# Kernel tuning notes

Measured on AMD Instinct MI355X. Metric: run time of the kernel, lower is better.

Reference implementation:

```python
import jax, jax.numpy as jnp
import numpy as np

J = 3
J_H = 5
C_IN = 128
C_OUT = 128
N0, N1, N2 = 1024, 3072, 2048
DENSITY = 0.01
W_SCALE = 0.02  # keeps P^(2^(J_h-1)) @ x @ W magnitudes reasonable in fp32


def _sym_sparse(key, n, density):
    kv, km = jax.random.split(key)
    mask = jax.random.uniform(km, (n, n)) < density
    a = jnp.where(mask, jax.random.normal(kv, (n, n)), 0.0)
    return jnp.triu(a) + jnp.triu(a, 1).T  # symmetric sparse 'Laplacian'


def _sparse(kv, km, shape, density):
    mask = jax.random.uniform(km, shape) < density
    return jnp.where(mask, jax.random.normal(kv, shape), 0.0)


def setup_inputs() -> dict:
    key = jax.random.key(0)
    ks = jax.random.split(key, 24)
    z0 = jax.random.normal(ks[0], (N0, C_IN), jnp.float32)
    z1 = jax.random.normal(ks[1], (N1, C_IN), jnp.float32)
    z2 = jax.random.normal(ks[2], (N2, C_IN), jnp.float32)
    L0 = _sym_sparse(ks[3], N0, 0.02)
    L1_d = _sym_sparse(ks[4], N1, DENSITY)
    L1_u = _sym_sparse(ks[5], N1, DENSITY)
    L2 = _sym_sparse(ks[6], N2, DENSITY)
    B1 = _sparse(ks[7], ks[8], (N0, N1), DENSITY)
    B2 = _sparse(ks[9], ks[10], (N1, N2), DENSITY)
    W_d = jax.random.normal(ks[11], (J, C_IN, C_OUT)) * W_SCALE
    W_u = jax.random.normal(ks[12], (J, C_IN, C_OUT)) * W_SCALE
    W_h = jax.random.normal(ks[13], (C_IN, C_OUT)) * W_SCALE
    W_b1 = jax.random.normal(ks[14], (J, C_IN, C_OUT)) * W_SCALE
    W_b2 = jax.random.normal(ks[15], (J, C_IN, C_OUT)) * W_SCALE
    attn_d_w = jax.random.normal(ks[16], (1, 2 * C_IN)) * W_SCALE
    attn_d_b = jax.random.normal(ks[17], (1,)) * W_SCALE
    attn_u_w = jax.random.normal(ks[18], (1, 2 * C_IN)) * W_SCALE
    attn_u_b = jax.random.normal(ks[19], (1,)) * W_SCALE
    return dict(z0=z0, z1=z1, z2=z2, L0=L0, L1_d=L1_d, L1_u=L1_u, L2=L2,
                B1=B1, B2=B2, W_d=W_d, W_u=W_u, W_h=W_h, W_b1=W_b1, W_b2=W_b2,
                attn_d_w=attn_d_w, attn_d_b=attn_d_b,
                attn_u_w=attn_u_w, attn_u_b=attn_u_b)


def _attention(x, n, w, b, src, dst):
    # gather edge endpoints -> tiny MLP -> sigmoid -> symmetric scatter
    a = jnp.concatenate([x[src], x[dst]], axis=-1)      # [E, 2C]
    s = jax.nn.sigmoid(a @ w.T + b)[:, 0]               # [E]
    return jnp.zeros((n, n), x.dtype).at[src, dst].set(s).at[dst, src].set(s)


def _harmonic(L, x, W_h):
    lmax = jnp.linalg.eigvalsh(L)[-1]
    # torch does lambda_max.item() -> constant w.r.t. grads
    eps = jax.lax.stop_gradient(jnp.where(lmax > 0, 1.0 / lmax, 0.1))
    P = jnp.eye(L.shape[0], dtype=x.dtype) - eps * L
    for _ in range(J_H - 1):
        P = P @ P                                        # P^(2^(J_h-1))
    return P @ x @ W_h


def reference(z0, z1, z2, L0, L1_d, L1_u, L2, B1, B2,
              W_d, W_u, W_h, W_b1, W_b2,
              attn_d_w, attn_d_b, attn_u_w, attn_u_b):
    # nonzero patterns of the Laplacians (constants, computed on host)
    src_d, dst_d = np.nonzero(np.asarray(jax.device_get(L1_d)))
    src_u, dst_u = np.nonzero(np.asarray(jax.device_get(L1_u)))
    L1d_attn = _attention(z1, N1, attn_d_w, attn_d_b,
                          jnp.asarray(src_d), jnp.asarray(dst_d))
    L1u_attn = _attention(z1, N1, attn_u_w, attn_u_b,
                          jnp.asarray(src_u), jnp.asarray(dst_u))
    # sum_j (A @ z) @ W[j] == (A @ z) @ W.sum(0)
    Wd_s, Wu_s = W_d.sum(0), W_u.sum(0)
    Wb1_s, Wb2_s = W_b1.sum(0), W_b2.sum(0)

    z0_out = (L0 @ z0) @ Wd_s + (B1 @ z1) @ Wb1_s + _harmonic(L0, z0, W_h)
    z0_out = jax.nn.relu(z0_out)

    z1_out = ((L1d_attn @ z1) @ Wd_s + (L1u_attn @ z1) @ Wu_s
              + (B1.T @ z0) @ Wb1_s + (B2 @ z2) @ Wb2_s
              + _harmonic(L1_d + L1_u, z1, W_h))
    z1_out = jax.nn.relu(z1_out)

    z2_out = (L2 @ z2) @ Wu_s + (B2.T @ z1) @ Wb2_s + _harmonic(L2, z2, W_h)
    z2_out = jax.nn.relu(z2_out)
    return (z0_out, z1_out, z2_out)
```

## Files before the change

### kernel.cpp

```cpp
#include <hip/hip_runtime.h>
#include <string.h>

constexpr int M_LZ = 48;

constexpr int CAP_L0 = 26240, CAP_L1 = 118016, CAP_L2 = 52480, CAP_B1 = 39360, CAP_B2 = 78720;
constexpr int CB_L0 = 0;
constexpr int CB_L1D = CB_L0 + CAP_L0;
constexpr int CB_L1U = CB_L1D + CAP_L1;
constexpr int CB_L2  = CB_L1U + CAP_L1;
constexpr int CB_B1  = CB_L2 + CAP_L2;
constexpr int CB_B2  = CB_B1 + CAP_B1;
constexpr int CAP_TOT= CB_B2 + CAP_B2;
constexpr int CB_B1T = CAP_TOT;
constexpr int CB_B2T = CB_B1T + CAP_B1;
constexpr int CAP_TOT2 = CB_B2T + CAP_B2;

constexpr int P_L0=0, P_L1D=1025, P_L1U=4098, P_L2=7171, P_B1=9220, P_B2=10245;
constexpr int P_B1T=13320, P_B2T=16393;
constexpr int C_L0=0, C_L1D=1024, C_L1U=4096, C_L2=7168, C_B1=9216, C_B2=10240;
constexpr int C_B1T=13312, C_B2T=16384;

constexpr size_t HBUF  = (size_t)6144*128;

constexpr size_t W_CNT = 0;
constexpr size_t W_PTR = 18432;
constexpr size_t W_CUR = W_PTR + 18444;
constexpr size_t W_CIDX= W_CUR + 5120;
constexpr size_t W_VAL = W_CIDX + CAP_TOT2;
constexpr size_t W_V0  = W_VAL + CAP_TOT2;
constexpr size_t W_PK  = W_V0 + 6144;
constexpr size_t W_TT  = W_PK + (size_t)64*6144*4;
constexpr size_t W_EPS = W_TT + 6144;
constexpr size_t W_UV  = W_EPS + 128;
constexpr size_t W_H   = W_UV + 4*3072;
constexpr size_t W_SCAT= W_H + 15*HBUF;
constexpr size_t S0_OFF= 0;
constexpr size_t S1_OFF= (size_t)1024*384;
constexpr size_t S2_OFF= S1_OFF + (size_t)3072*640;
constexpr size_t SCAT_TOT = S2_OFF + (size_t)2048*384;
constexpr size_t W_WCAT= W_SCAT + SCAT_TOT;
constexpr size_t WC0=0, WC1=(size_t)384*128, WC2=WC1+(size_t)640*128;
constexpr size_t W_SLOT= W_WCAT + (size_t)1408*128;
constexpr size_t W_FLG = W_SLOT + 1048576;
constexpr size_t W_REL = W_FLG + 65536;

__device__ __forceinline__ float wredf(float v){
  #pragma unroll
  for(int o=32;o;o>>=1) v += __shfl_xor(v,o,64);
  return v;
}
__device__ __forceinline__ int wredi(int v){
  #pragma unroll
  for(int o=32;o;o>>=1) v += __shfl_xor(v,o,64);
  return v;
}
__device__ __forceinline__ void red4x2(float4& a0, float4& a1){
  #pragma unroll
  for (int o=16;o<=32;o<<=1){
    a0.x+=__shfl_xor(a0.x,o,64); a0.y+=__shfl_xor(a0.y,o,64);
    a0.z+=__shfl_xor(a0.z,o,64); a0.w+=__shfl_xor(a0.w,o,64);
    a1.x+=__shfl_xor(a1.x,o,64); a1.y+=__shfl_xor(a1.y,o,64);
    a1.z+=__shfl_xor(a1.z,o,64); a1.w+=__shfl_xor(a1.w,o,64);
  }
}
__device__ __forceinline__ float v0hash(int i, float invs){
  unsigned uu=(unsigned)i*2654435761u; uu^=uu>>16; uu*=2246822519u; uu^=uu>>13;
  return (uu&1)?invs:-invs;
}

__device__ __forceinline__ float ldc(const float* p){
  return __hip_atomic_load(p, __ATOMIC_RELAXED, __HIP_MEMORY_SCOPE_AGENT);
}
__device__ __forceinline__ float2 ldc2(const float* p){
  unsigned long long u = __hip_atomic_load((const unsigned long long*)p,
                          __ATOMIC_RELAXED, __HIP_MEMORY_SCOPE_AGENT);
  float2 r; memcpy(&r,&u,8); return r;
}
__device__ __forceinline__ void stc(float* p, float v){
  __hip_atomic_store(p, v, __ATOMIC_RELAXED, __HIP_MEMORY_SCOPE_AGENT);
}
__device__ __forceinline__ void stc2(float* p, float2 v){
  unsigned long long u; memcpy(&u,&v,8);
  __hip_atomic_store((unsigned long long*)p, u, __ATOMIC_RELAXED, __HIP_MEMORY_SCOPE_AGENT);
}
__device__ __forceinline__ int ldci(const int* p){
  return __hip_atomic_load(p, __ATOMIC_RELAXED, __HIP_MEMORY_SCOPE_AGENT);
}
__device__ __forceinline__ void stci(int* p, int v){
  __hip_atomic_store(p, v, __ATOMIC_RELAXED, __HIP_MEMORY_SCOPE_AGENT);
}

__device__ __forceinline__ void barg(float* ws, int* leafs, int b, int lbase, int Ng,
                                     bool chk, int lidx, int ph){
  const int t = threadIdx.x;
  int* flg = (int*)ws + W_FLG;
  __builtin_amdgcn_s_waitcnt(0);
  __syncthreads();
  if (t==0) stci(flg + (size_t)b*32, ph+1);
  if (chk){
    for (int s=t; s<Ng; s+=256){
      const int* f = flg + (size_t)(lbase+s)*32;
      while (ldci(f) < ph+1) __builtin_amdgcn_s_sleep(1);
    }
    __syncthreads();
    if (t==0){
      #pragma unroll
      for (int i=0;i<16;i++) stci(leafs + (size_t)i*32, ph+1);
    }
    __syncthreads();
  } else {
    if (t==0){
      const int* rl = leafs + (size_t)(lidx&15)*32;
      while (ldci(rl) < ph+1) __builtin_amdgcn_s_sleep(1);
    }
    __syncthreads();
  }
}

__device__ __forceinline__ void bar_lz(float* ws, int b, int grp, int lbase, int Lg,
                                       bool chk, int lb, int ph, int j,
                                       float* shr, float* redm,
                                       float& a_o, float& g_o, float& ib_o){
  const int t = threadIdx.x, lane = t&63, wvv = t>>6;
  __builtin_amdgcn_s_waitcnt(0);
  __syncthreads();
  if (t==0){
    float A0=redm[0]+redm[1]+redm[2]+redm[3];
    float G0=redm[4]+redm[5]+redm[6]+redm[7];
    float N0=redm[8]+redm[9]+redm[10]+redm[11];
    float* sl = ws + W_SLOT + ((size_t)j*2048 + b)*8;
    stc2(sl+2, make_float2(A0,G0)); stc(sl+4, N0);
    __builtin_amdgcn_s_waitcnt(0);
    stci((int*)sl, ph+1);
  }
  if (chk){
    float pa=0.f, pg=0.f, pn=0.f;
    for (int s=t; s<Lg; s+=256){
      const float* sl = ws + W_SLOT + ((size_t)j*2048 + lbase+s)*8;
      while (ldci((const int*)sl) < ph+1) __builtin_amdgcn_s_sleep(1);
      float2 ag = ldc2(sl+2); float nn = ldc(sl+4);
      pa+=ag.x; pg+=ag.y; pn+=nn;
    }
    pa=wredf(pa); pg=wredf(pg); pn=wredf(pn);
    if (lane==0){ shr[0*4+wvv]=pa; shr[1*4+wvv]=pg; shr[2*4+wvv]=pn; }
    __syncthreads();
    if (t==0){
      float a=shr[0]+shr[1]+shr[2]+shr[3];
      float g=shr[4]+shr[5]+shr[6]+shr[7];
      float n=shr[8]+shr[9]+shr[10]+shr[11];
      float ib = 1.f/sqrtf(fmaxf(n - a*a - g*g, 1e-20f));
      float* TT = ws + W_TT + (size_t)(grp*64 + j)*32;
      stc2(TT, make_float2(a,g)); stc(TT+2, n);
      #pragma unroll
      for (int i=0;i<16;i++){
        float* lf = ws + W_REL + (size_t)(grp*16+i)*32;
        stc2(lf+2, make_float2(a,g)); stc(lf+4, ib);
      }
      __builtin_amdgcn_s_waitcnt(0);
      #pragma unroll
      for (int i=0;i<16;i++)
        stci((int*)(ws + W_REL) + (size_t)(grp*16+i)*32, ph+1);
      shr[0]=a; shr[1]=g; shr[2]=ib;
    }
    __syncthreads();
  } else {
    if (t==0){
      const float* lf = ws + W_REL + (size_t)(grp*16 + (lb&15))*32;
      while (ldci((const int*)lf) < ph+1) __builtin_amdgcn_s_sleep(1);
      float2 ag = ldc2(lf+2); float ib = ldc(lf+4);
      shr[0]=ag.x; shr[1]=ag.y; shr[2]=ib;
    }
    __syncthreads();
  }
  a_o = shr[0]; g_o = shr[1]; ib_o = shr[2];
}

__global__ void k_wprep(const float* Wd,const float* Wu,const float* Wh,
                        const float* Wb1,const float* Wb2, float* ws){
  int t = blockIdx.x*256 + threadIdx.x;
  if (t >= 16384) return;
  int* wsi = (int*)ws;
  if (t < 5120) wsi[W_CNT + 13312 + t] = 0;
  if (t < 5120) wsi[W_CUR + t] = 0;
  for (int i=t; i<65536+2048; i+=16384) wsi[W_FLG+i] = 0;
  for (int i=t; i<131072; i+=16384) wsi[W_SLOT + (size_t)i*8] = 0;
  float sd = Wd[t]  + Wd[16384+t]  + Wd[32768+t];
  float su = Wu[t]  + Wu[16384+t]  + Wu[32768+t];
  float s1 = Wb1[t] + Wb1[16384+t] + Wb1[32768+t];
  float s2 = Wb2[t] + Wb2[16384+t] + Wb2[32768+t];
  float wh = Wh[t];
  float* W0 = ws + W_WCAT + WC0;
  float* W1 = ws + W_WCAT + WC1;
  float* W2 = ws + W_WCAT + WC2;
  W0[t]=sd; W0[16384+t]=s1; W0[32768+t]=wh;
  W1[t]=sd; W1[16384+t]=su; W1[32768+t]=s1; W1[49152+t]=s2; W1[65536+t]=wh;
  W2[t]=su; W2[16384+t]=s2; W2[32768+t]=wh;
}

__device__ __forceinline__ void mat_meta(int wid, const float* L0,const float* L1d,const float* L1u,
    const float* L2,const float* B1,const float* B2,
    const float*& M,int& ncol,int& lrow,int& co,int& po,int& cb,int& cap,int& tco){
  if (wid < 1024){ M=L0;  ncol=1024; lrow=wid;        co=C_L0;  po=P_L0;  cb=CB_L0;  cap=CAP_L0; tco=-1; }
  else if (wid < 4096){ M=L1d; ncol=3072; lrow=wid-1024;  co=C_L1D; po=P_L1D; cb=CB_L1D; cap=CAP_L1; tco=-1; }
  else if (wid < 7168){ M=L1u; ncol=3072; lrow=wid-4096;  co=C_L1U; po=P_L1U; cb=CB_L1U; cap=CAP_L1; tco=-1; }
  else if (wid < 9216){ M=L2;  ncol=2048; lrow=wid-7168;  co=C_L2;  po=P_L2;  cb=CB_L2;  cap=CAP_L2; tco=-1; }
  else if (wid < 10240){ M=B1; ncol=3072; lrow=wid-9216;  co=C_B1;  po=P_B1;  cb=CB_B1;  cap=CAP_B1; tco=C_B1T; }
  else { M=B2; ncol=2048; lrow=wid-10240; co=C_B2;  po=P_B2;  cb=CB_B2;  cap=CAP_B2; tco=C_B2T; }
}

__global__ void k_count(const float* L0,const float* L1d,const float* L1u,const float* L2,
                        const float* B1,const float* B2,int* cnt){
  int wid = blockIdx.x*4 + (threadIdx.x>>6);
  int lane = threadIdx.x & 63;
  if (wid >= 13312) return;
  const float* M; int ncol,lrow,co,po,cb,cap,tco;
  mat_meta(wid,L0,L1d,L1u,L2,B1,B2,M,ncol,lrow,co,po,cb,cap,tco);
  const float4* row4 = (const float4*)(M + (size_t)lrow*ncol);
  int c = 0;
  for (int j0=0; j0<ncol; j0+=256){
    float4 v = row4[(j0>>2)+lane];
    int n0=v.x!=0.f, n1=v.y!=0.f, n2=v.z!=0.f, n3=v.w!=0.f;
    c += n0+n1+n2+n3;
    if (tco>=0){
      int jb = j0 + lane*4;
      if (n0) atomicAdd(cnt+tco+jb,   1);
      if (n1) atomicAdd(cnt+tco+jb+1, 1);
      if (n2) atomicAdd(cnt+tco+jb+2, 1);
      if (n3) atomicAdd(cnt+tco+jb+3, 1);
    }
  }
  c = wredi(c);
  if (lane==0) cnt[co+lrow] = c;
}

__global__ void k_prefix(const int* cnt, int* ptr, int* cur){
  __shared__ int lds[257];
  const int rows[8]={1024,3072,3072,2048,1024,3072,3072,2048};
  const int cofs[8]={C_L0,C_L1D,C_L1U,C_L2,C_B1,C_B2,C_B1T,C_B2T};
  const int pofs[8]={P_L0,P_L1D,P_L1U,P_L2,P_B1,P_B2,P_B1T,P_B2T};
  int b=blockIdx.x, t=threadIdx.x;
  int R=rows[b]; const int* c=cnt+cofs[b]; int* p=ptr+pofs[b];
  int* cc = (b==6)? cur : (b==7)? cur+3072 : nullptr;
  int chunk=(R+255)/256;
  int lo=t*chunk, hi=min(R,lo+chunk);
  int s=0;
  for(int i=lo;i<hi;i++) s+=c[i];
  lds[t]=s; __syncthreads();
  if(t==0){ int run=0; for(int i=0;i<256;i++){int x=lds[i];lds[i]=run;run+=x;} lds[256]=run; }
  __syncthreads();
  int run=lds[t];
  for(int i=lo;i<hi;i++){ p[i]=run; if(cc) cc[i]=run; run+=c[i]; }
  if(t==0) p[R]=lds[256];
}

__global__ void k_fill(const float* L0,const float* L1d,const float* L1u,const float* L2,
                       const float* B1,const float* B2,const int* ptr,int* cidx,float* val){
  int wid = blockIdx.x*4 + (threadIdx.x>>6);
  int lane = threadIdx.x & 63;
  if (wid >= 13312) return;
  const float* M; int ncol,lrow,co,po,cb,cap,tco;
  mat_meta(wid,L0,L1d,L1u,L2,B1,B2,M,ncol,lrow,co,po,cb,cap,tco);
  const float4* row4 = (const float4*)(M + (size_t)lrow*ncol);
  int base = ptr[po+lrow];
  int run = 0;
  for (int j0=0; j0<ncol; j0+=256){
    float4 v = row4[(j0>>2)+lane];
    int n0=v.x!=0.f, n1=v.y!=0.f, n2=v.z!=0.f, n3=v.w!=0.f;
    int local = n0+n1+n2+n3;
    int incl = local;
    #pragma unroll
    for (int o=1;o<64;o<<=1){
      int tmp = __shfl_up(incl,o,64);
      if (lane>=o) incl += tmp;
    }
    int tot = __shfl(incl,63,64);
    int pos = base + run + incl - local;
    int jb = j0 + lane*4;
    if (n0){ if(pos<cap){cidx[cb+pos]=jb;   val[cb+pos]=v.x;} pos++; }
    if (n1){ if(pos<cap){cidx[cb+pos]=jb+1; val[cb+pos]=v.y;} pos++; }
    if (n2){ if(pos<cap){cidx[cb+pos]=jb+2; val[cb+pos]=v.z;} pos++; }
    if (n3){ if(pos<cap){cidx[cb+pos]=jb+3; val[cb+pos]=v.w;} pos++; }
    run += tot;
  }
}

__global__ void k_fillT(float* ws){
  int wid = blockIdx.x*4 + (threadIdx.x>>6);
  int lane = threadIdx.x & 63;
  if (wid >= 4096) return;
  int* wsi=(int*)ws;
  const int* ptr=wsi+W_PTR; int* cidx=wsi+W_CIDX; float* val=ws+W_VAL;
  int* cur=wsi+W_CUR;
  if (wid < 1024){
    int r=wid;
    int e=ptr[P_B1+r+1];
    for(int k=ptr[P_B1+r]+lane;k<e;k+=64){
      int c=cidx[CB_B1+k]; float v=val[CB_B1+k];
      int pos=atomicAdd(cur+c,1);
      cidx[CB_B1T+pos]=r; val[CB_B1T+pos]=v;
    }
  } else {
    int r=wid-1024;
    int e=ptr[P_B2+r+1];
    for(int k=ptr[P_B2+r]+lane;k<e;k+=64){
      int c=cidx[CB_B2+k]; float v=val[CB_B2+k];
      int pos=atomicAdd(cur+3072+c,1);
      cidx[CB_B2T+pos]=r; val[CB_B2T+pos]=v;
    }
  }
}

__global__ __launch_bounds__(256,8) void k_solve(float* ws,
    const float* z0,const float* z1,const float* z2,
    const float* adw,const float* adb,const float* auw,const float* aub,
    float* out){
  const int b = blockIdx.x, t = threadIdx.x;
  const int wv = t>>6, lane = t&63;
  const int sg = lane>>4, chn = lane&15;
  const int* wsi=(const int*)ws;
  const int* ptr=wsi+W_PTR; const int* cidx=wsi+W_CIDX; const float* val=ws+W_VAL;

  __shared__ float smem[2616];
  float* Sl  = smem;
  float* Wl  = smem + 544;
  float* TTa = smem;
  float* TTb = smem + 64;
  float* redm= smem + 2592;
  float* shr = smem + 2604;

  int* grel = (int*)ws + W_REL + 48*32;
  int* krel = (int*)ws + W_SLOT + 63*2048*8;

  if (b < 768){
    int g, gbase, nb;
    if (b<128){ g=0; gbase=0;   nb=0;    }
    else if (b<512){ g=1; gbase=128; nb=1024; }
    else { g=2; gbase=512; nb=4096; }
    const int lb = b - gbase;
    const int Lg = (g==0)?128:(g==1)?384:256;
    const bool chk = (lb==0);
    const float invsg = (g==0)?0.03125f:(g==1)?0.0180421959f:0.0220970869f;
    const int hw = lane>>5, hl = lane&31;
    const int p  = lb*8 + wv*2 + hw;
    const int gp = nb + p;
    float a=0.f, gmm=0.f, ib=1.f;
    float vp_m1=0.f, vp_m2=0.f, wp_m1=0.f;
    for (int j=0;j<M_LZ;j++){
      float wp=0.f;
      if (j==0){
        #define GZ(PP,CBB) { const int* rp=ptr+PP; int e=rp[p+1]; \
          for (int k=rp[p]+hl;k<e;k+=32){ wp += val[CBB+k]*v0hash(nb+cidx[CBB+k], invsg); } }
        if (g==0){ GZ(P_L0,CB_L0) }
        else if (g==1){ GZ(P_L1D,CB_L1D) GZ(P_L1U,CB_L1U) }
        else { GZ(P_L2,CB_L2) }
        #undef GZ
      } else {
        const float4* pk = (const float4*)(ws + W_PK) + (size_t)(j-1)*6144 + nb;
        #define GP(PP,CBB) { const int* rp=ptr+PP; int e=rp[p+1]; \
          for (int k=rp[p]+hl;k<e;k+=32){ float v=val[CBB+k]; float4 pq=pk[cidx[CBB+k]]; \
            wp += v*((pq.x - a*pq.y - gmm*pq.z)*ib); } }
        if (g==0){ GP(P_L0,CB_L0) }
        else if (g==1){ GP(P_L1D,CB_L1D) GP(P_L1U,CB_L1U) }
        else { GP(P_L2,CB_L2) }
        #undef GP
      }
      #pragma unroll
      for (int o=16;o;o>>=1) wp += __shfl_xor(wp,o,64);
      float rA=0.f, rG=0.f, rN=0.f;
      if (hl==0){
        float vp;
        if (j==0) vp = v0hash(gp, invsg);
        else      vp = (wp_m1 - a*vp_m1 - gmm*vp_m2)*ib;
        float* pkw = ws + W_PK + ((size_t)j*6144 + gp)*4;
        stc2(pkw, make_float2(wp, vp)); stc(pkw+2, vp_m1);
        rA = vp*wp; rG = vp_m1*wp; rN = wp*wp;
        vp_m2 = vp_m1; vp_m1 = vp; wp_m1 = wp;
      }
      rA += __shfl_xor(rA,32,64); rG += __shfl_xor(rG,32,64); rN += __shfl_xor(rN,32,64);
      if (lane==0){ redm[0*4+wv]=rA; redm[1*4+wv]=rG; redm[2*4+wv]=rN; }
      bar_lz(ws, b, g, gbase, Lg, chk, lb, 1+j, j, shr, redm, a, gmm, ib);
    }
    if (chk && t<64){
      int i = t;
      double lo=1e300, hi=-1e300;
      if (i<M_LZ){
        const float* TT = ws + W_TT + (size_t)(g*64 + i)*32;
        float aa=TT[0], gg=TT[1], nn=TT[2];
        TTa[i]=aa; TTb[i]=sqrtf(fmaxf(nn-aa*aa-gg*gg,1e-20f));
      }
      if (i<M_LZ){
        double r=(i? fabs((double)TTb[i-1]):0.0) + (i<M_LZ-1? fabs((double)TTb[i]):0.0);
        lo=(double)TTa[i]-r; hi=(double)TTa[i]+r;
      }
      #pragma unroll
      for(int o=32;o;o>>=1){ lo=fmin(lo,__shfl_xor(lo,o,64)); hi=fmax(hi,__shfl_xor(hi,o,64)); }
      lo -= 1.0; hi += 1.0;
      for (int round=0; round<4; round++){
        double x = lo + (hi-lo)*(double)(i+1)/65.0;
        double d = 1.0; int cnt2=0;
        for (int k2=0;k2<M_LZ;k2++){
          double bi = k2? (double)TTb[k2-1] : 0.0;
          d = ((double)TTa[k2]-x) - bi*bi/d;
          if (d==0.0) d = -1e-300;
          if (d<0.0) cnt2++;
        }
        double nlo = (cnt2< M_LZ)? x : -1e300;
        double nhi = (cnt2==M_LZ)? x :  1e300;
        #pragma unroll
        for(int o=32;o;o>>=1){ nlo=fmax(nlo,__shfl_xor(nlo,o,64)); nhi=fmin(nhi,__shfl_xor(nhi,o,64)); }
        if (nlo>-1e299) lo=nlo;
        if (nhi< 1e299) hi=nhi;
      }
      double lam = 0.5*(lo+hi);
      if (i==0) stc(ws+W_EPS+(size_t)g*32, (lam>0.0)? (float)(1.0/lam) : 0.1f);
    }
  } else {
    const int kb = b - 768;
    const int vw = kb*4 + wv;
    if (vw < 3072){
      float2 x  = ((const float2*)(z1+(size_t)vw*128))[lane];
      float2 a0 = ((const float2*)adw)[lane];
      float2 a1 = ((const float2*)adw)[64+lane];
      float2 b0 = ((const float2*)auw)[lane];
      float2 b1 = ((const float2*)auw)[64+lane];
      float ud=x.x*a0.x+x.y*a0.y, vd=x.x*a1.x+x.y*a1.y;
      float uu=x.x*b0.x+x.y*b0.y, vu=x.x*b1.x+x.y*b1.y;
      ud=wredf(ud); vd=wredf(vd); uu=wredf(uu); vu=wredf(vu);
      if(lane==0){ stc(ws+W_UV+vw,ud); stc(ws+W_UV+3072+vw,vd);
                   stc(ws+W_UV+6144+vw,uu); stc(ws+W_UV+9216+vw,vu); }
    }
    int cgP, nbP, lrP; float e0P;
    if (vw < 3072){ cgP=1; nbP=1024; lrP=vw;      e0P=(1.f/28.f); }
    else          { cgP=2; nbP=4096; lrP=vw-3072; e0P=0.0625f;    }
    const bool has2 = (vw >= 4096);
    const int lr2 = vw - 4096;
    for (int k2=1; k2<=16; k2++){
      const float* ybase = ws + W_H + (size_t)(k2>=2? k2-2:0)*HBUF;
      #define KG2(PP,CBB,NBV,ZZV,LRV) { const int* rp=ptr+PP; int e=rp[(LRV)+1]; \
        for (int kk=rp[LRV]+sg; kk<e; kk+=4){ \
          float v=val[CBB+kk]; int q=cidx[CBB+kk]; \
          const float* sr = (k2==1)? (ZZV)+(size_t)q*128 : ybase+(size_t)((NBV)+q)*128; \
          float4 x0=((const float4*)sr)[chn*2], x1=((const float4*)sr)[chn*2+1]; \
          a0.x+=v*x0.x; a0.y+=v*x0.y; a0.z+=v*x0.z; a0.w+=v*x0.w; \
          a1.x+=v*x1.x; a1.y+=v*x1.y; a1.z+=v*x1.z; a1.w+=v*x1.w; \
        } }
      #define KWRITE(CGV,LRV,GRV,E0V) if (lane<16){ \
          float* dst; \
          if (k2<16) dst = ws + W_H + (size_t)(k2-1)*HBUF + (size_t)(GRV)*128; \
          else { \
            if ((CGV)==0)      dst = ws+W_SCAT+S0_OFF+256 + (size_t)(LRV)*384; \
            else if ((CGV)==1) dst = ws+W_SCAT+S1_OFF+512 + (size_t)(LRV)*640; \
            else               dst = ws+W_SCAT+S2_OFF+256 + (size_t)(LRV)*384; \
          } \
          stc2(dst+chn*8,   make_float2((E0V)*a0.x, (E0V)*a0.y)); \
          stc2(dst+chn*8+2, make_float2((E0V)*a0.z, (E0V)*a0.w)); \
          stc2(dst+chn*8+4, make_float2((E0V)*a1.x, (E0V)*a1.y)); \
          stc2(dst+chn*8+6, make_float2((E0V)*a1.z, (E0V)*a1.w)); }
      {
        float4 a0={0.f,0.f,0.f,0.f}, a1={0.f,0.f,0.f,0.f};
        if (cgP==1){ KG2(P_L1D,CB_L1D,1024,z1,lrP) KG2(P_L1U,CB_L1U,1024,z1,lrP) }
        else { KG2(P_L2,CB_L2,4096,z2,lrP) }
        red4x2(a0,a1);
        KWRITE(cgP, lrP, nbP+lrP, e0P)
      }
      if (has2){
        float4 a0={0.f,0.f,0.f,0.f}, a1={0.f,0.f,0.f,0.f};
        KG2(P_L0,CB_L0,0,z0,lr2)
        red4x2(a0,a1);
        KWRITE(0, lr2, lr2, 0.0625f)
      }
      #undef KG2
      #undef KWRITE
      if (k2<16) barg(ws, krel, b, 768, 1280, b==768, kb, k2);
    }
    for (int wid2 = kb*4+wv; wid2 < 18432; wid2 += 5120){
      int task,p2;
      if(wid2<1024){task=0;p2=wid2;}
      else if(wid2<2048){task=1;p2=wid2-1024;}
      else if(wid2<5120){task=2;p2=wid2-2048;}
      else if(wid2<8192){task=3;p2=wid2-5120;}
      else if(wid2<11264){task=4;p2=wid2-8192;}
      else if(wid2<13312){task=5;p2=wid2-11264;}
      else if(wid2<16384){task=6;p2=wid2-13312;}
      else {task=7;p2=wid2-16384;}
      const float* in; const int* rp; int cb2; float* outp; int ostride;
      int mode=0; float Vp=0.f, bb=0.f; const float* U=nullptr;
      switch(task){
        case 0: rp=ptr+P_L0;  cb2=CB_L0;  in=z0; outp=ws+W_SCAT+S0_OFF+0;   ostride=384; break;
        case 1: rp=ptr+P_B1;  cb2=CB_B1;  in=z1; outp=ws+W_SCAT+S0_OFF+128; ostride=384; break;
        case 2: rp=ptr+P_L1D; cb2=CB_L1D; in=z1; outp=ws+W_SCAT+S1_OFF+0;   ostride=640;
                mode=1; U=ws+W_UV; Vp=ws[W_UV+3072+p2]; bb=adb[0]; break;
        case 3: rp=ptr+P_L1U; cb2=CB_L1U; in=z1; outp=ws+W_SCAT+S1_OFF+128; ostride=640;
                mode=1; U=ws+W_UV+6144; Vp=ws[W_UV+9216+p2]; bb=aub[0]; break;
        case 4: rp=ptr+P_B2;  cb2=CB_B2;  in=z2; outp=ws+W_SCAT+S1_OFF+384; ostride=640; break;
        case 5: rp=ptr+P_L2;  cb2=CB_L2;  in=z2; outp=ws+W_SCAT+S2_OFF+0;   ostride=384; break;
        case 6: rp=ptr+P_B1T; cb2=CB_B1T; in=z0; outp=ws+W_SCAT+S1_OFF+256; ostride=640; break;
        default:rp=ptr+P_B2T; cb2=CB_B2T; in=z1; outp=ws+W_SCAT+S2_OFF+128; ostride=384; break;
      }
      float4 a0={0.f,0.f,0.f,0.f}, a1={0.f,0.f,0.f,0.f};
      int e=rp[p2+1];
      for (int k=rp[p2]+sg; k<e; k+=4){
        int q = cidx[cb2+k];
        float v;
        if (mode) v = 1.0f/(1.0f+__expf(-(U[q]+Vp+bb)));
        else v = val[cb2+k];
        const float* sr = in + (size_t)q*128;
        float4 x0 = ((const float4*)sr)[chn*2];
        float4 x1 = ((const float4*)sr)[chn*2+1];
        a0.x+=v*x0.x; a0.y+=v*x0.y; a0.z+=v*x0.z; a0.w+=v*x0.w;
        a1.x+=v*x1.x; a1.y+=v*x1.y; a1.z+=v*x1.z; a1.w+=v*x1.w;
      }
      red4x2(a0, a1);
      if (sg==0){
        float* dst = outp + (size_t)p2*ostride;
        stc2(dst+chn*8,   make_float2(a0.x,a0.y));
        stc2(dst+chn*8+2, make_float2(a0.z,a0.w));
        stc2(dst+chn*8+4, make_float2(a1.x,a1.y));
        stc2(dst+chn*8+6, make_float2(a1.z,a1.w));
      }
    }
  }

  barg(ws, grel, b, 0, 2048, b==1, b, 30);

  { int r = b*4+wv;
    if (r < 6144){
      int cg = (r<1024)?0:(r<4096)?1:2;
      int lr = r - ((cg==0)?0:(cg==1)?1024:4096);
      const float* zz = (cg==0)?z0:(cg==1)?z1:z2;
      float lam0 = (cg==1)?28.f:16.f;
      float eps  = ws[W_EPS+(size_t)cg*32];
      float rr = eps*lam0;
      float* hc;
      if (cg==0)      hc = ws+W_SCAT+S0_OFF+256 + (size_t)lr*384;
      else if (cg==1) hc = ws+W_SCAT+S1_OFF+512 + (size_t)lr*640;
      else            hc = ws+W_SCAT+S2_OFF+256 + (size_t)lr*384;
      const float BIN[17] = {1.f,16.f,120.f,560.f,1820.f,4368.f,8008.f,11440.f,12870.f,
                             11440.f,8008.f,4368.f,1820.f,560.f,120.f,16.f,1.f};
      float2 acc = ((const float2*)(zz + (size_t)lr*128))[lane];
      float rk = 1.f;
      #pragma unroll
      for (int k2=1;k2<=15;k2++){
        rk *= -rr;
        float2 y = ((const float2*)(ws + W_H + (size_t)(k2-1)*HBUF + (size_t)r*128))[lane];
        float c = BIN[k2]*rk;
        acc.x += c*y.x; acc.y += c*y.y;
      }
      rk *= -rr;
      float2 y16 = ((const float2*)hc)[lane];
      acc.x += rk*y16.x; acc.y += rk*y16.y;
      stc2(hc + (size_t)lane*2, acc);
    }
  }
  barg(ws, grel, b, 0, 2048, b==1, b, 31);

  if (b < 192){
    const float* S; const float* W; float* outp; int K; int blk;
    if (b<32){       S=ws+W_SCAT+S0_OFF; W=ws+W_WCAT+WC0; outp=out;        K=384; blk=b; }
    else if (b<128){ S=ws+W_SCAT+S1_OFF; W=ws+W_WCAT+WC1; outp=out+131072; K=640; blk=b-32; }
    else {           S=ws+W_SCAT+S2_OFF; W=ws+W_WCAT+WC2; outp=out+524288; K=384; blk=b-128; }
    int r0=blk*32;
    int ty=t>>5, tx=t&31;
    float acc[4][4]={};
    for (int k0=0; k0<K; k0+=16){
      {
        int r=t>>3, kq=(t&7)*2;
        const float* src=S+(size_t)(r0+r)*K + k0+kq;
        Sl[r*17+kq]=src[0]; Sl[r*17+kq+1]=src[1];
      }
      {
        int kk=t>>4, cq=(t&15)*8;
        const float* src=W+(size_t)(k0+kk)*128+cq;
        #pragma unroll
        for(int i=0;i<8;i++) Wl[kk*128+cq+i]=src[i];
      }
      __syncthreads();
      #pragma unroll
      for(int k=0;k<16;k++){
        float sv[4], wvv2[4];
        #pragma unroll
        for(int i=0;i<4;i++) sv[i]=Sl[(ty*4+i)*17+k];
        #pragma unroll
        for(int i=0;i<4;i++) wvv2[i]=Wl[k*128+tx+32*i];
        #pragma unroll
        for(int a2=0;a2<4;a2++)
          #pragma unroll
          for(int b2=0;b2<4;b2++) acc[a2][b2]+=sv[a2]*wvv2[b2];
      }
      __syncthreads();
    }
    #pragma unroll
    for(int a2=0;a2<4;a2++)
      #pragma unroll
      for(int b2=0;b2<4;b2++){
        int r=r0+ty*4+a2, col=tx+32*b2;
        outp[(size_t)r*128+col]=fmaxf(acc[a2][b2],0.f);
      }
  }
}

extern "C" void kernel_launch(void* const* d_in, const int* in_sizes, int n_in,
                              void* d_out, int out_size, void* d_ws, size_t ws_size,
                              hipStream_t stream){
  const float* z0 =(const float*)d_in[0];
  const float* z1 =(const float*)d_in[1];
  const float* z2 =(const float*)d_in[2];
  const float* L0 =(const float*)d_in[3];
  const float* L1d=(const float*)d_in[4];
  const float* L1u=(const float*)d_in[5];
  const float* L2 =(const float*)d_in[6];
  const float* B1 =(const float*)d_in[7];
  const float* B2 =(const float*)d_in[8];
  const float* Wd =(const float*)d_in[9];
  const float* Wu =(const float*)d_in[10];
  const float* Wh =(const float*)d_in[11];
  const float* Wb1=(const float*)d_in[12];
  const float* Wb2=(const float*)d_in[13];
  const float* adw=(const float*)d_in[14];
  const float* adb=(const float*)d_in[15];
  const float* auw=(const float*)d_in[16];
  const float* aub=(const float*)d_in[17];
  float* ws=(float*)d_ws;
  int* wsi=(int*)d_ws;
  float* out=(float*)d_out;

  hipLaunchKernelGGL(k_wprep, dim3(64), dim3(256), 0, stream, Wd,Wu,Wh,Wb1,Wb2,ws);
  hipLaunchKernelGGL(k_count, dim3(3328), dim3(256), 0, stream, L0,L1d,L1u,L2,B1,B2, wsi+W_CNT);
  hipLaunchKernelGGL(k_prefix, dim3(8), dim3(256), 0, stream, wsi+W_CNT, wsi+W_PTR, wsi+W_CUR);
  hipLaunchKernelGGL(k_fill, dim3(3328), dim3(256), 0, stream, L0,L1d,L1u,L2,B1,B2, wsi+W_PTR, wsi+W_CIDX, ws+W_VAL);
  hipLaunchKernelGGL(k_fillT, dim3(1024), dim3(256), 0, stream, ws);
  hipLaunchKernelGGL(k_solve, dim3(2048), dim3(256), 0, stream,
                     ws, z0, z1, z2, adw, adb, auw, aub, out);
}
```

Before: 780.1 us.

## Fuse sparse count and fill into single-pass extraction with atomic row bases

Replaces the count, prefix and fill kernels with one k_extract kernel. It reads each dense matrix row once, stages its nonzeros in LDS (capped at 128 per row) and takes a row base offset from a per-matrix atomic counter. Rows are now stored as (start, count) pairs in arbitrary order rather than as a prefix-sum CSR, and every consumer is changed to read start plus count. This removes one full pass over the dense matrices, which dominate memory traffic, and the serial prefix kernel. The cost is nondeterministic row placement, a 128-nonzero-per-row cap that silently truncates denser rows, and a small added k_tbase kernel for the transpose bases.

```diff
diff --git a/kernel.cpp b/kernel.cpp
--- a/kernel.cpp
+++ b/kernel.cpp
@@ -181,7 +181,7 @@
   if (t >= 16384) return;
   int* wsi = (int*)ws;
   if (t < 5120) wsi[W_CNT + 13312 + t] = 0;
-  if (t < 5120) wsi[W_CUR + t] = 0;
+  if (t < 8)    wsi[W_V0 + (size_t)t*32] = 0;
   for (int i=t; i<65536+2048; i+=16384) wsi[W_FLG+i] = 0;
   for (int i=t; i<131072; i+=16384) wsi[W_SLOT + (size_t)i*8] = 0;
   float sd = Wd[t]  + Wd[16384+t]  + Wd[32768+t];
@@ -199,69 +199,32 @@
 
 __device__ __forceinline__ void mat_meta(int wid, const float* L0,const float* L1d,const float* L1u,
     const float* L2,const float* B1,const float* B2,
-    const float*& M,int& ncol,int& lrow,int& co,int& po,int& cb,int& cap,int& tco){
-  if (wid < 1024){ M=L0;  ncol=1024; lrow=wid;        co=C_L0;  po=P_L0;  cb=CB_L0;  cap=CAP_L0; tco=-1; }
-  else if (wid < 4096){ M=L1d; ncol=3072; lrow=wid-1024;  co=C_L1D; po=P_L1D; cb=CB_L1D; cap=CAP_L1; tco=-1; }
-  else if (wid < 7168){ M=L1u; ncol=3072; lrow=wid-4096;  co=C_L1U; po=P_L1U; cb=CB_L1U; cap=CAP_L1; tco=-1; }
-  else if (wid < 9216){ M=L2;  ncol=2048; lrow=wid-7168;  co=C_L2;  po=P_L2;  cb=CB_L2;  cap=CAP_L2; tco=-1; }
-  else if (wid < 10240){ M=B1; ncol=3072; lrow=wid-9216;  co=C_B1;  po=P_B1;  cb=CB_B1;  cap=CAP_B1; tco=C_B1T; }
-  else { M=B2; ncol=2048; lrow=wid-10240; co=C_B2;  po=P_B2;  cb=CB_B2;  cap=CAP_B2; tco=C_B2T; }
-}
-
-__global__ void k_count(const float* L0,const float* L1d,const float* L1u,const float* L2,
-                        const float* B1,const float* B2,int* cnt){
+    const float*& M,int& ncol,int& lrow,int& co,int& po,int& cb,int& cap,int& tco,int& mi){
+  if (wid < 1024){ M=L0;  ncol=1024; lrow=wid;        co=C_L0;  po=P_L0;  cb=CB_L0;  cap=CAP_L0; tco=-1; mi=0; }
+  else if (wid < 4096){ M=L1d; ncol=3072; lrow=wid-1024;  co=C_L1D; po=P_L1D; cb=CB_L1D; cap=CAP_L1; tco=-1; mi=1; }
+  else if (wid < 7168){ M=L1u; ncol=3072; lrow=wid-4096;  co=C_L1U; po=P_L1U; cb=CB_L1U; cap=CAP_L1; tco=-1; mi=2; }
+  else if (wid < 9216){ M=L2;  ncol=2048; lrow=wid-7168;  co=C_L2;  po=P_L2;  cb=CB_L2;  cap=CAP_L2; tco=-1; mi=3; }
+  else if (wid < 10240){ M=B1; ncol=3072; lrow=wid-9216;  co=C_B1;  po=P_B1;  cb=CB_B1;  cap=CAP_B1; tco=C_B1T; mi=4; }
+  else { M=B2; ncol=2048; lrow=wid-10240; co=C_B2;  po=P_B2;  cb=CB_B2;  cap=CAP_B2; tco=C_B2T; mi=5; }
+}
+
+__global__ void k_extract(const float* L0,const float* L1d,const float* L1u,const float* L2,
+                          const float* B1,const float* B2, float* ws){
+  int* wsi=(int*)ws;
+  int* cnt = wsi + W_CNT;
+  int* ptrb= wsi + W_PTR;
+  int* cidx= wsi + W_CIDX;
+  float* val= ws + W_VAL;
+  int* curM= wsi + W_V0;
+  __shared__ int   sidx[4][128];
+  __shared__ float sval[4][128];
   int wid = blockIdx.x*4 + (threadIdx.x>>6);
   int lane = threadIdx.x & 63;
+  int wv = threadIdx.x>>6;
   if (wid >= 13312) return;
-  const float* M; int ncol,lrow,co,po,cb,cap,tco;
-  mat_meta(wid,L0,L1d,L1u,L2,B1,B2,M,ncol,lrow,co,po,cb,cap,tco);
+  const float* M; int ncol,lrow,co,po,cb,cap,tco,mi;
+  mat_meta(wid,L0,L1d,L1u,L2,B1,B2,M,ncol,lrow,co,po,cb,cap,tco,mi);
   const float4* row4 = (const float4*)(M + (size_t)lrow*ncol);
-  int c = 0;
-  for (int j0=0; j0<ncol; j0+=256){
-    float4 v = row4[(j0>>2)+lane];
-    int n0=v.x!=0.f, n1=v.y!=0.f, n2=v.z!=0.f, n3=v.w!=0.f;
-    c += n0+n1+n2+n3;
-    if (tco>=0){
-      int jb = j0 + lane*4;
-      if (n0) atomicAdd(cnt+tco+jb,   1);
-      if (n1) atomicAdd(cnt+tco+jb+1, 1);
-      if (n2) atomicAdd(cnt+tco+jb+2, 1);
-      if (n3) atomicAdd(cnt+tco+jb+3, 1);
-    }
-  }
-  c = wredi(c);
-  if (lane==0) cnt[co+lrow] = c;
-}
-
-__global__ void k_prefix(const int* cnt, int* ptr, int* cur){
-  __shared__ int lds[257];
-  const int rows[8]={1024,3072,3072,2048,1024,3072,3072,2048};
-  const int cofs[8]={C_L0,C_L1D,C_L1U,C_L2,C_B1,C_B2,C_B1T,C_B2T};
-  const int pofs[8]={P_L0,P_L1D,P_L1U,P_L2,P_B1,P_B2,P_B1T,P_B2T};
-  int b=blockIdx.x, t=threadIdx.x;
-  int R=rows[b]; const int* c=cnt+cofs[b]; int* p=ptr+pofs[b];
-  int* cc = (b==6)? cur : (b==7)? cur+3072 : nullptr;
-  int chunk=(R+255)/256;
-  int lo=t*chunk, hi=min(R,lo+chunk);
-  int s=0;
-  for(int i=lo;i<hi;i++) s+=c[i];
-  lds[t]=s; __syncthreads();
-  if(t==0){ int run=0; for(int i=0;i<256;i++){int x=lds[i];lds[i]=run;run+=x;} lds[256]=run; }
-  __syncthreads();
-  int run=lds[t];
-  for(int i=lo;i<hi;i++){ p[i]=run; if(cc) cc[i]=run; run+=c[i]; }
-  if(t==0) p[R]=lds[256];
-}
-
-__global__ void k_fill(const float* L0,const float* L1d,const float* L1u,const float* L2,
-                       const float* B1,const float* B2,const int* ptr,int* cidx,float* val){
-  int wid = blockIdx.x*4 + (threadIdx.x>>6);
-  int lane = threadIdx.x & 63;
-  if (wid >= 13312) return;
-  const float* M; int ncol,lrow,co,po,cb,cap,tco;
-  mat_meta(wid,L0,L1d,L1u,L2,B1,B2,M,ncol,lrow,co,po,cb,cap,tco);
-  const float4* row4 = (const float4*)(M + (size_t)lrow*ncol);
-  int base = ptr[po+lrow];
   int run = 0;
   for (int j0=0; j0<ncol; j0+=256){
     float4 v = row4[(j0>>2)+lane];
@@ -274,14 +237,45 @@
       if (lane>=o) incl += tmp;
     }
     int tot = __shfl(incl,63,64);
-    int pos = base + run + incl - local;
+    int pos = run + incl - local;
     int jb = j0 + lane*4;
-    if (n0){ if(pos<cap){cidx[cb+pos]=jb;   val[cb+pos]=v.x;} pos++; }
-    if (n1){ if(pos<cap){cidx[cb+pos]=jb+1; val[cb+pos]=v.y;} pos++; }
-    if (n2){ if(pos<cap){cidx[cb+pos]=jb+2; val[cb+pos]=v.z;} pos++; }
-    if (n3){ if(pos<cap){cidx[cb+pos]=jb+3; val[cb+pos]=v.w;} pos++; }
+    if (n0){ if(pos<128){sidx[wv][pos]=jb;   sval[wv][pos]=v.x;} pos++; }
+    if (n1){ if(pos<128){sidx[wv][pos]=jb+1; sval[wv][pos]=v.y;} pos++; }
+    if (n2){ if(pos<128){sidx[wv][pos]=jb+2; sval[wv][pos]=v.z;} pos++; }
+    if (n3){ if(pos<128){sidx[wv][pos]=jb+3; sval[wv][pos]=v.w;} pos++; }
+    if (tco>=0){
+      if (n0) atomicAdd(cnt+tco+jb,   1);
+      if (n1) atomicAdd(cnt+tco+jb+1, 1);
+      if (n2) atomicAdd(cnt+tco+jb+2, 1);
+      if (n3) atomicAdd(cnt+tco+jb+3, 1);
+    }
     run += tot;
   }
+  int rn = min(run,128);
+  int base = 0;
+  if (lane==0){
+    base = atomicAdd(curM + mi*32, rn);
+    ptrb[po+lrow] = base;
+    cnt[co+lrow]  = rn;
+  }
+  base = __shfl(base,0,64);
+  for (int k=lane; k<rn; k+=64){
+    int q = base+k;
+    if (q<cap){ cidx[cb+q]=sidx[wv][k]; val[cb+q]=sval[wv][k]; }
+  }
+}
+
+__global__ void k_tbase(float* ws){
+  int t = blockIdx.x*256 + threadIdx.x;
+  if (t >= 5120) return;
+  int* wsi=(int*)ws;
+  int* cnt=wsi+W_CNT; int* ptrb=wsi+W_PTR; int* cur=wsi+W_CUR;
+  int* curM=wsi+W_V0;
+  int c = cnt[13312+t];
+  int base;
+  if (t<3072){ base=atomicAdd(curM+6*32, c); ptrb[P_B1T+t]=base; }
+  else       { base=atomicAdd(curM+7*32, c); ptrb[P_B2T+(t-3072)]=base; }
+  cur[t]=base;
 }
 
 __global__ void k_fillT(float* ws){
@@ -289,20 +283,21 @@
   int lane = threadIdx.x & 63;
   if (wid >= 4096) return;
   int* wsi=(int*)ws;
-  const int* ptr=wsi+W_PTR; int* cidx=wsi+W_CIDX; float* val=ws+W_VAL;
+  const int* ptr=wsi+W_PTR; const int* cn=wsi+W_CNT;
+  int* cidx=wsi+W_CIDX; float* val=ws+W_VAL;
   int* cur=wsi+W_CUR;
   if (wid < 1024){
     int r=wid;
-    int e=ptr[P_B1+r+1];
-    for(int k=ptr[P_B1+r]+lane;k<e;k+=64){
+    int s0=ptr[P_B1+r]; int e=s0+cn[C_B1+r];
+    for(int k=s0+lane;k<e;k+=64){
       int c=cidx[CB_B1+k]; float v=val[CB_B1+k];
       int pos=atomicAdd(cur+c,1);
       cidx[CB_B1T+pos]=r; val[CB_B1T+pos]=v;
     }
   } else {
     int r=wid-1024;
-    int e=ptr[P_B2+r+1];
-    for(int k=ptr[P_B2+r]+lane;k<e;k+=64){
+    int s0=ptr[P_B2+r]; int e=s0+cn[C_B2+r];
+    for(int k=s0+lane;k<e;k+=64){
       int c=cidx[CB_B2+k]; float v=val[CB_B2+k];
       int pos=atomicAdd(cur+3072+c,1);
       cidx[CB_B2T+pos]=r; val[CB_B2T+pos]=v;
@@ -318,7 +313,8 @@
   const int wv = t>>6, lane = t&63;
   const int sg = lane>>4, chn = lane&15;
   const int* wsi=(const int*)ws;
-  const int* ptr=wsi+W_PTR; const int* cidx=wsi+W_CIDX; const float* val=ws+W_VAL;
+  const int* ptr=wsi+W_PTR; const int* cn=wsi+W_CNT;
+  const int* cidx=wsi+W_CIDX; const float* val=ws+W_VAL;
 
   __shared__ float smem[2616];
   float* Sl  = smem;
@@ -348,20 +344,20 @@
     for (int j=0;j<M_LZ;j++){
       float wp=0.f;
       if (j==0){
-        #define GZ(PP,CBB) { const int* rp=ptr+PP; int e=rp[p+1]; \
-          for (int k=rp[p]+hl;k<e;k+=32){ wp += val[CBB+k]*v0hash(nb+cidx[CBB+k], invsg); } }
-        if (g==0){ GZ(P_L0,CB_L0) }
-        else if (g==1){ GZ(P_L1D,CB_L1D) GZ(P_L1U,CB_L1U) }
-        else { GZ(P_L2,CB_L2) }
+        #define GZ(PP,CO,CBB) { int s0=ptr[(PP)+p]; int e=s0+cn[(CO)+p]; \
+          for (int k=s0+hl;k<e;k+=32){ wp += val[CBB+k]*v0hash(nb+cidx[CBB+k], invsg); } }
+        if (g==0){ GZ(P_L0,C_L0,CB_L0) }
+        else if (g==1){ GZ(P_L1D,C_L1D,CB_L1D) GZ(P_L1U,C_L1U,CB_L1U) }
+        else { GZ(P_L2,C_L2,CB_L2) }
         #undef GZ
       } else {
         const float4* pk = (const float4*)(ws + W_PK) + (size_t)(j-1)*6144 + nb;
-        #define GP(PP,CBB) { const int* rp=ptr+PP; int e=rp[p+1]; \
-          for (int k=rp[p]+hl;k<e;k+=32){ float v=val[CBB+k]; float4 pq=pk[cidx[CBB+k]]; \
+        #define GP(PP,CO,CBB) { int s0=ptr[(PP)+p]; int e=s0+cn[(CO)+p]; \
+          for (int k=s0+hl;k<e;k+=32){ float v=val[CBB+k]; float4 pq=pk[cidx[CBB+k]]; \
             wp += v*((pq.x - a*pq.y - gmm*pq.z)*ib); } }
-        if (g==0){ GP(P_L0,CB_L0) }
-        else if (g==1){ GP(P_L1D,CB_L1D) GP(P_L1U,CB_L1U) }
-        else { GP(P_L2,CB_L2) }
+        if (g==0){ GP(P_L0,C_L0,CB_L0) }
+        else if (g==1){ GP(P_L1D,C_L1D,CB_L1D) GP(P_L1U,C_L1U,CB_L1U) }
+        else { GP(P_L2,C_L2,CB_L2) }
         #undef GP
       }
       #pragma unroll
@@ -436,8 +432,8 @@
     const int lr2 = vw - 4096;
     for (int k2=1; k2<=16; k2++){
       const float* ybase = ws + W_H + (size_t)(k2>=2? k2-2:0)*HBUF;
-      #define KG2(PP,CBB,NBV,ZZV,LRV) { const int* rp=ptr+PP; int e=rp[(LRV)+1]; \
-        for (int kk=rp[LRV]+sg; kk<e; kk+=4){ \
+      #define KG2(PP,CO,CBB,NBV,ZZV,LRV) { int s0=ptr[(PP)+(LRV)]; int e=s0+cn[(CO)+(LRV)]; \
+        for (int kk=s0+sg; kk<e; kk+=4){ \
           float v=val[CBB+kk]; int q=cidx[CBB+kk]; \
           const float* sr = (k2==1)? (ZZV)+(size_t)q*128 : ybase+(size_t)((NBV)+q)*128; \
           float4 x0=((const float4*)sr)[chn*2], x1=((const float4*)sr)[chn*2+1]; \
@@ -458,14 +454,14 @@
           stc2(dst+chn*8+6, make_float2((E0V)*a1.z, (E0V)*a1.w)); }
       {
         float4 a0={0.f,0.f,0.f,0.f}, a1={0.f,0.f,0.f,0.f};
-        if (cgP==1){ KG2(P_L1D,CB_L1D,1024,z1,lrP) KG2(P_L1U,CB_L1U,1024,z1,lrP) }
-        else { KG2(P_L2,CB_L2,4096,z2,lrP) }
+        if (cgP==1){ KG2(P_L1D,C_L1D,CB_L1D,1024,z1,lrP) KG2(P_L1U,C_L1U,CB_L1U,1024,z1,lrP) }
+        else { KG2(P_L2,C_L2,CB_L2,4096,z2,lrP) }
         red4x2(a0,a1);
         KWRITE(cgP, lrP, nbP+lrP, e0P)
       }
       if (has2){
         float4 a0={0.f,0.f,0.f,0.f}, a1={0.f,0.f,0.f,0.f};
-        KG2(P_L0,CB_L0,0,z0,lr2)
+        KG2(P_L0,C_L0,CB_L0,0,z0,lr2)
         red4x2(a0,a1);
         KWRITE(0, lr2, lr2, 0.0625f)
       }
@@ -483,23 +479,23 @@
       else if(wid2<13312){task=5;p2=wid2-11264;}
       else if(wid2<16384){task=6;p2=wid2-13312;}
       else {task=7;p2=wid2-16384;}
-      const float* in; const int* rp; int cb2; float* outp; int ostride;
+      const float* in; const int* rp; int co2, cb2; float* outp; int ostride;
       int mode=0; float Vp=0.f, bb=0.f; const float* U=nullptr;
       switch(task){
-        case 0: rp=ptr+P_L0;  cb2=CB_L0;  in=z0; outp=ws+W_SCAT+S0_OFF+0;   ostride=384; break;
-        case 1: rp=ptr+P_B1;  cb2=CB_B1;  in=z1; outp=ws+W_SCAT+S0_OFF+128; ostride=384; break;
-        case 2: rp=ptr+P_L1D; cb2=CB_L1D; in=z1; outp=ws+W_SCAT+S1_OFF+0;   ostride=640;
+        case 0: rp=ptr+P_L0;  co2=C_L0;  cb2=CB_L0;  in=z0; outp=ws+W_SCAT+S0_OFF+0;   ostride=384; break;
+        case 1: rp=ptr+P_B1;  co2=C_B1;  cb2=CB_B1;  in=z1; outp=ws+W_SCAT+S0_OFF+128; ostride=384; break;
+        case 2: rp=ptr+P_L1D; co2=C_L1D; cb2=CB_L1D; in=z1; outp=ws+W_SCAT+S1_OFF+0;   ostride=640;
                 mode=1; U=ws+W_UV; Vp=ws[W_UV+3072+p2]; bb=adb[0]; break;
-        case 3: rp=ptr+P_L1U; cb2=CB_L1U; in=z1; outp=ws+W_SCAT+S1_OFF+128; ostride=640;
+        case 3: rp=ptr+P_L1U; co2=C_L1U; cb2=CB_L1U; in=z1; outp=ws+W_SCAT+S1_OFF+128; ostride=640;
                 mode=1; U=ws+W_UV+6144; Vp=ws[W_UV+9216+p2]; bb=aub[0]; break;
-        case 4: rp=ptr+P_B2;  cb2=CB_B2;  in=z2; outp=ws+W_SCAT+S1_OFF+384; ostride=640; break;
-        case 5: rp=ptr+P_L2;  cb2=CB_L2;  in=z2; outp=ws+W_SCAT+S2_OFF+0;   ostride=384; break;
-        case 6: rp=ptr+P_B1T; cb2=CB_B1T; in=z0; outp=ws+W_SCAT+S1_OFF+256; ostride=640; break;
-        default:rp=ptr+P_B2T; cb2=CB_B2T; in=z1; outp=ws+W_SCAT+S2_OFF+128; ostride=384; break;
+        case 4: rp=ptr+P_B2;  co2=C_B2;  cb2=CB_B2;  in=z2; outp=ws+W_SCAT+S1_OFF+384; ostride=640; break;
+        case 5: rp=ptr+P_L2;  co2=C_L2;  cb2=CB_L2;  in=z2; outp=ws+W_SCAT+S2_OFF+0;   ostride=384; break;
+        case 6: rp=ptr+P_B1T; co2=C_B1T; cb2=CB_B1T; in=z0; outp=ws+W_SCAT+S1_OFF+256; ostride=640; break;
+        default:rp=ptr+P_B2T; co2=C_B2T; cb2=CB_B2T; in=z1; outp=ws+W_SCAT+S2_OFF+128; ostride=384; break;
       }
       float4 a0={0.f,0.f,0.f,0.f}, a1={0.f,0.f,0.f,0.f};
-      int e=rp[p2+1];
-      for (int k=rp[p2]+sg; k<e; k+=4){
+      int s0=rp[p2]; int e=s0+cn[co2+p2];
+      for (int k=s0+sg; k<e; k+=4){
         int q = cidx[cb2+k];
         float v;
         if (mode) v = 1.0f/(1.0f+__expf(-(U[q]+Vp+bb)));
@@ -621,13 +617,11 @@
   const float* auw=(const float*)d_in[16];
   const float* aub=(const float*)d_in[17];
   float* ws=(float*)d_ws;
-  int* wsi=(int*)d_ws;
   float* out=(float*)d_out;
 
   hipLaunchKernelGGL(k_wprep, dim3(64), dim3(256), 0, stream, Wd,Wu,Wh,Wb1,Wb2,ws);
-  hipLaunchKernelGGL(k_count, dim3(3328), dim3(256), 0, stream, L0,L1d,L1u,L2,B1,B2, wsi+W_CNT);
-  hipLaunchKernelGGL(k_prefix, dim3(8), dim3(256), 0, stream, wsi+W_CNT, wsi+W_PTR, wsi+W_CUR);
-  hipLaunchKernelGGL(k_fill, dim3(3328), dim3(256), 0, stream, L0,L1d,L1u,L2,B1,B2, wsi+W_PTR, wsi+W_CIDX, ws+W_VAL);
+  hipLaunchKernelGGL(k_extract, dim3(3328), dim3(256), 0, stream, L0,L1d,L1u,L2,B1,B2, ws);
+  hipLaunchKernelGGL(k_tbase, dim3(20), dim3(256), 0, stream, ws);
   hipLaunchKernelGGL(k_fillT, dim3(1024), dim3(256), 0, stream, ws);
   hipLaunchKernelGGL(k_solve, dim3(2048), dim3(256), 0, stream,
                      ws, z0, z1, z2, adw, adb, auw, aub, out);
```

New measurement: 808.5 us. 3.7% more time.
